# Optimization experiments

Measured on AMD Instinct MI355X. Metric: run time of the kernel, lower is better.

Reference implementation:

```python
import jax, jax.numpy as jnp
import numpy as np

B, N, H, DH, CZ = 1, 768, 16, 32, 128
D = H * DH  # 512
EPS = 1e-5


def layer_norm(x, w, b):
    mu = jnp.mean(x, axis=-1, keepdims=True)
    var = jnp.var(x, axis=-1, keepdims=True)
    return (x - mu) * jax.lax.rsqrt(var + EPS) * w + b


def setup_inputs() -> dict:
    key = jax.random.key(0)
    ks = jax.random.split(key, 10)
    sc = 0.02
    return {
        "s": jax.random.normal(ks[0], (B, N, D), jnp.float32),
        "z": jax.random.normal(ks[1], (B, N, N, CZ), jnp.float32),
        "norm_s_w": jnp.ones((D,), jnp.float32),
        "norm_s_b": jnp.zeros((D,), jnp.float32),
        "q_w": jax.random.normal(ks[2], (D, D), jnp.float32) * sc,
        "q_b": jax.random.normal(ks[3], (D,), jnp.float32) * sc,
        "k_w": jax.random.normal(ks[4], (D, D), jnp.float32) * sc,
        "v_w": jax.random.normal(ks[5], (D, D), jnp.float32) * sc,
        "g_w": jax.random.normal(ks[6], (D, D), jnp.float32) * sc,
        "zn_w": jnp.ones((CZ,), jnp.float32),
        "zn_b": jnp.zeros((CZ,), jnp.float32),
        "z_w": jax.random.normal(ks[7], (CZ, H), jnp.float32) * sc,
        "o_w": jax.random.normal(ks[8], (D, D), jnp.float32) * sc,
    }


def reference(s, z, norm_s_w, norm_s_b, q_w, q_b, k_w, v_w, g_w, zn_w, zn_b, z_w, o_w):
    # initial_norm on s
    s_n = layer_norm(s, norm_s_w, norm_s_b)
    # QKV projections (q has bias, k/v do not)
    q = (s_n @ q_w + q_b).reshape(B, N, H, DH)
    k = (s_n @ k_w).reshape(B, N, H, DH)
    v = (s_n @ v_w).reshape(B, N, H, DH)
    # attention scores [B, H, N, N]
    scores = jnp.einsum("bihd,bjhd->bhij", q, k) * (DH ** -0.5)
    # pair bias: layernorm(z) then linear c_z -> H, permute to [B, H, N, N]
    z_bias = layer_norm(z, zn_w, zn_b) @ z_w            # [B, N, N, H]
    z_bias = jnp.transpose(z_bias, (0, 3, 1, 2))         # [B, H, N, N]
    a = jax.nn.softmax(scores + z_bias, axis=-1)
    # attend
    o = jnp.einsum("bhij,bjhd->bihd", a, v).reshape(B, N, D)
    # sigmoid gate from normed s
    g = jax.nn.sigmoid(s_n @ g_w)
    # output projection
    return (o * g) @ o_w
```

## Files before the change

### kernel.cpp

```cpp
#include <hip/hip_runtime.h>
#include <hip/hip_bf16.h>

typedef float f32x4 __attribute__((ext_vector_type(4)));
typedef short bf16x8 __attribute__((ext_vector_type(8)));
typedef unsigned short u16;

#define NTOK 768
#define DMOD 512
#define NH   16
#define DH   32
#define CZd  128
#define NN   (768*768)

static __device__ __forceinline__ u16 f2bf(float f) {
  __hip_bfloat16 h = __float2bfloat16(f);
  return __builtin_bit_cast(u16, h);
}
static __device__ __forceinline__ float bf2f(u16 u) {
  unsigned int x = ((unsigned int)u) << 16;
  return __builtin_bit_cast(float, x);
}

__global__ __launch_bounds__(256) void prep_kernel(
    const float* __restrict__ s, const float* __restrict__ nsw, const float* __restrict__ nsb,
    const float* __restrict__ qw, const float* __restrict__ kw, const float* __restrict__ vw,
    const float* __restrict__ gw, const float* __restrict__ ow,
    const float* __restrict__ z, const float* __restrict__ znw, const float* __restrict__ znb,
    const float* __restrict__ zwp,
    u16* __restrict__ wbf, u16* __restrict__ snb, u16* __restrict__ biasb) {
  __shared__ char SM[17408];
  int bid = blockIdx.x;
  int t = threadIdx.x;

  if (bid >= 9216) {
    if (bid < 10496) {
      float (*tbuf)[33] = (float(*)[33])SM;
      int wb = bid - 9216;
      int seg = wb / 256;
      int tile = wb % 256;
      int k0 = (tile / 16) * 32;
      int n0 = (tile % 16) * 32;
      const float* src = seg==0?qw: seg==1?kw: seg==2?vw: seg==3?gw: ow;
      u16* out = wbf + (size_t)seg * (DMOD*DMOD);
      int tr  = t / 8;
      int tc4 = (t % 8) * 4;
      float4 v = *(const float4*)(src + (size_t)(k0+tr)*DMOD + n0 + tc4);
      tbuf[tr][tc4+0]=v.x; tbuf[tr][tc4+1]=v.y; tbuf[tr][tc4+2]=v.z; tbuf[tr][tc4+3]=v.w;
      __syncthreads();
      int nr  = t / 8;
      int kc4 = (t % 8) * 4;
      ushort4 o;
      o.x = f2bf(tbuf[kc4+0][nr]);
      o.y = f2bf(tbuf[kc4+1][nr]);
      o.z = f2bf(tbuf[kc4+2][nr]);
      o.w = f2bf(tbuf[kc4+3][nr]);
      *(ushort4*)(out + (size_t)(n0+nr)*DMOD + k0 + kc4) = o;
    } else {
      int i = (bid - 10496)*4 + (t >> 6);
      int lane = t & 63;
      const float* row = s + (size_t)i*DMOD + lane*8;
      float4 a0 = *(const float4*)(row);
      float4 a1 = *(const float4*)(row + 4);
      float sum = a0.x+a0.y+a0.z+a0.w + a1.x+a1.y+a1.z+a1.w;
      float sq  = a0.x*a0.x+a0.y*a0.y+a0.z*a0.z+a0.w*a0.w
                + a1.x*a1.x+a1.y*a1.y+a1.z*a1.z+a1.w*a1.w;
      #pragma unroll
      for (int mk=1; mk<64; mk<<=1) { sum += __shfl_xor(sum,mk); sq += __shfl_xor(sq,mk); }
      float mu  = sum * (1.f/512.f);
      float var = sq  * (1.f/512.f) - mu*mu;
      float rs  = rsqrtf(var + 1e-5f);
      float4 w0 = *(const float4*)(nsw + lane*8);
      float4 w1 = *(const float4*)(nsw + lane*8 + 4);
      float4 b0 = *(const float4*)(nsb + lane*8);
      float4 b1 = *(const float4*)(nsb + lane*8 + 4);
      bf16x8 o;
      o[0]=(short)f2bf((a0.x-mu)*rs*w0.x+b0.x);
      o[1]=(short)f2bf((a0.y-mu)*rs*w0.y+b0.y);
      o[2]=(short)f2bf((a0.z-mu)*rs*w0.z+b0.z);
      o[3]=(short)f2bf((a0.w-mu)*rs*w0.w+b0.w);
      o[4]=(short)f2bf((a1.x-mu)*rs*w1.x+b1.x);
      o[5]=(short)f2bf((a1.y-mu)*rs*w1.y+b1.y);
      o[6]=(short)f2bf((a1.z-mu)*rs*w1.z+b1.z);
      o[7]=(short)f2bf((a1.w-mu)*rs*w1.w+b1.w);
      *(bf16x8*)(snb + (size_t)i*DMOD + lane*8) = o;
    }
    return;
  }

  u16* zt = (u16*)SM;
  int i = bid / 12, j0 = (bid % 12) * 64;
  int lane = t & 63, wv = t >> 6;
  int c16 = lane & 15, c4 = lane >> 4;
  int rsub = t >> 5;
  int ch4  = (t & 31) * 4;
  const float* ztile = z + ((size_t)i*NTOK + j0)*CZd;
  float4 xv[8];
  #pragma unroll
  for (int it=0; it<8; it++)
    xv[it] = *(const float4*)(ztile + (size_t)(it*8 + rsub)*CZd + ch4);
  bf16x8 bfr[4];
  #pragma unroll
  for (int ks=0; ks<4; ks++) {
    #pragma unroll
    for (int jj=0; jj<8; jj++)
      bfr[ks][jj] = (short)f2bf(zwp[(ks*32 + c4*8 + jj)*16 + c16]);
  }
  float4 w4 = *(const float4*)(znw + ch4);
  float4 b4 = *(const float4*)(znb + ch4);
  float mu8[8], rs8[8];
  #pragma unroll
  for (int it=0; it<8; it++) {
    float4 v = xv[it];
    float sum = v.x+v.y+v.z+v.w;
    float sq  = v.x*v.x+v.y*v.y+v.z*v.z+v.w*v.w;
    #pragma unroll
    for (int mk=1; mk<32; mk<<=1) { sum += __shfl_xor(sum,mk); sq += __shfl_xor(sq,mk); }
    float mu = sum*(1.f/128.f);
    mu8[it] = mu;
    rs8[it] = rsqrtf(sq*(1.f/128.f) - mu*mu + 1e-5f);
  }
  #pragma unroll
  for (int it=0; it<8; it++) {
    float4 v = xv[it];
    float mu = mu8[it], rs = rs8[it];
    ushort4 o;
    o.x = f2bf((v.x-mu)*rs*w4.x + b4.x);
    o.y = f2bf((v.y-mu)*rs*w4.y + b4.y);
    o.z = f2bf((v.z-mu)*rs*w4.z + b4.z);
    o.w = f2bf((v.w-mu)*rs*w4.w + b4.w);
    *(ushort4*)(zt + (it*8 + rsub)*136 + ch4) = o;
  }
  __syncthreads();
  f32x4 acc = {0,0,0,0};
  #pragma unroll
  for (int ks=0; ks<4; ks++) {
    bf16x8 af = *(const bf16x8*)(zt + (wv*16 + c16)*136 + ks*32 + c4*8);
    acc = __builtin_amdgcn_mfma_f32_16x16x32_bf16(af, bfr[ks], acc, 0,0,0);
  }
  int jl = j0 + wv*16 + c4*4;
  u16* bp = biasb + ((size_t)i*NH + c16)*NTOK + jl;
  ushort4 st;
  st.x = f2bf(acc[0]); st.y = f2bf(acc[1]); st.z = f2bf(acc[2]); st.w = f2bf(acc[3]);
  *(ushort4*)bp = st;
}

__global__ __launch_bounds__(256) void qkvg_kernel(
    const u16* __restrict__ sn, const u16* __restrict__ wts, const float* __restrict__ qb,
    u16* __restrict__ qo, u16* __restrict__ ko, u16* __restrict__ vTo, float* __restrict__ go) {
  int bid = blockIdx.x;
  int mb = bid % 24, nb = bid / 24;
  int wsel = nb >> 3, n0 = (nb & 7) * 64, m0 = mb * 32;
  const u16* wt = wts + (size_t)wsel * (DMOD*DMOD);
  int t = threadIdx.x, lane = t & 63, wv = t >> 6;
  int wm = (wv >> 1) * 16, wn = (wv & 1) * 32;
  int c16 = lane & 15, c4 = lane >> 4;
  const u16* arow  = sn + (size_t)(m0 + wm + c16)*DMOD + c4*8;
  const u16* brow0 = wt + (size_t)(n0 + wn + c16)*DMOD + c4*8;
  const u16* brow1 = wt + (size_t)(n0 + wn + 16 + c16)*DMOD + c4*8;
  f32x4 acc0={0,0,0,0}, acc1={0,0,0,0};
  #pragma unroll 4
  for (int k0 = 0; k0 < DMOD; k0 += 32) {
    bf16x8 a  = *(const bf16x8*)(arow  + k0);
    bf16x8 b0 = *(const bf16x8*)(brow0 + k0);
    bf16x8 b1 = *(const bf16x8*)(brow1 + k0);
    acc0 = __builtin_amdgcn_mfma_f32_16x16x32_bf16(a,b0,acc0,0,0,0);
    acc1 = __builtin_amdgcn_mfma_f32_16x16x32_bf16(a,b1,acc1,0,0,0);
  }
  int r0 = c4*4;
  #pragma unroll
  for (int bn=0; bn<2; bn++) {
    f32x4 acc = bn==0?acc0:acc1;
    #pragma unroll
    for (int rr=0; rr<4; rr++) {
      int i = m0 + wm + r0 + rr;
      int n = n0 + wn + bn*16 + c16;
      float val = acc[rr];
      if (wsel == 0)      { val += qb[n]; qo[(size_t)i*DMOD + n] = f2bf(val); }
      else if (wsel == 1) { ko[(size_t)i*DMOD + n] = f2bf(val); }
      else if (wsel == 2) { vTo[(size_t)n*NTOK + i] = f2bf(val); }
      else                { go[(size_t)i*DMOD + n] = 1.f/(1.f + expf(-val)); }
    }
  }
}

__global__ __launch_bounds__(256) void attn_kernel(
    const u16* __restrict__ qm, const u16* __restrict__ km, const u16* __restrict__ vTm,
    const u16* __restrict__ bias, const float* __restrict__ gm, u16* __restrict__ og) {
  __shared__ u16 Pt[4][16*72];
  __shared__ float OS[4][16][33];
  __shared__ float LS[4][16];
  int h  = blockIdx.x & 15;
  int i0 = (blockIdx.x >> 4) * 16;
  int t = threadIdx.x, lane = t & 63, wv = t >> 6;
  int c16 = lane & 15, c4 = lane >> 4, r0 = c4 * 4;
  bf16x8 qf = *(const bf16x8*)(qm + (size_t)(i0 + c16)*DMOD + h*DH + c4*8);
  f32x4 o0 = {0,0,0,0}, o1 = {0,0,0,0};
  float ls[4] = {0.f,0.f,0.f,0.f};
  const float scale = 0.17677669529663687f;
  const u16* bbase = bias + ((size_t)i0*NH + h)*NTOK;
  u16* pt = &Pt[wv][0];
  for (int jj = 0; jj < 3; jj++) {
    int j0 = wv*192 + jj*64;
    bf16x8 kf0 = *(const bf16x8*)(km + (size_t)(j0 +  0 + c16)*DMOD + h*DH + c4*8);
    bf16x8 kf1 = *(const bf16x8*)(km + (size_t)(j0 + 16 + c16)*DMOD + h*DH + c4*8);
    bf16x8 kf2 = *(const bf16x8*)(km + (size_t)(j0 + 32 + c16)*DMOD + h*DH + c4*8);
    bf16x8 kf3 = *(const bf16x8*)(km + (size_t)(j0 + 48 + c16)*DMOD + h*DH + c4*8);
    f32x4 zz = {0,0,0,0};
    f32x4 s0 = __builtin_amdgcn_mfma_f32_16x16x32_bf16(qf,kf0,zz,0,0,0);
    f32x4 s1 = __builtin_amdgcn_mfma_f32_16x16x32_bf16(qf,kf1,zz,0,0,0);
    f32x4 s2 = __builtin_amdgcn_mfma_f32_16x16x32_bf16(qf,kf2,zz,0,0,0);
    f32x4 s3 = __builtin_amdgcn_mfma_f32_16x16x32_bf16(qf,kf3,zz,0,0,0);
    #pragma unroll
    for (int rr=0; rr<4; rr++) {
      const u16* bp = bbase + (size_t)(r0+rr)*(NH*NTOK) + j0 + c16;
      int row = (r0 + rr) * 72;
      float p0 = __expf(s0[rr]*scale + bf2f(bp[ 0]));
      float p1 = __expf(s1[rr]*scale + bf2f(bp[16]));
      float p2 = __expf(s2[rr]*scale + bf2f(bp[32]));
      float p3 = __expf(s3[rr]*scale + bf2f(bp[48]));
      ls[rr] += p0 + p1 + p2 + p3;
      pt[row + 0*16 + c16] = f2bf(p0);
      pt[row + 1*16 + c16] = f2bf(p1);
      pt[row + 2*16 + c16] = f2bf(p2);
      pt[row + 3*16 + c16] = f2bf(p3);
    }
    #pragma unroll
    for (int ks=0; ks<2; ks++) {
      bf16x8 pf = *(const bf16x8*)(pt + c16*72 + ks*32 + c4*8);
      bf16x8 v0 = *(const bf16x8*)(vTm + (size_t)(h*DH + c16)*NTOK      + j0 + ks*32 + c4*8);
      bf16x8 v1 = *(const bf16x8*)(vTm + (size_t)(h*DH + 16 + c16)*NTOK + j0 + ks*32 + c4*8);
      o0 = __builtin_amdgcn_mfma_f32_16x16x32_bf16(pf, v0, o0, 0,0,0);
      o1 = __builtin_amdgcn_mfma_f32_16x16x32_bf16(pf, v1, o1, 0,0,0);
    }
  }
  #pragma unroll
  for (int rr=0; rr<4; rr++) {
    float l = ls[rr];
    l += __shfl_xor(l,1); l += __shfl_xor(l,2); l += __shfl_xor(l,4); l += __shfl_xor(l,8);
    OS[wv][r0+rr][c16]      = o0[rr];
    OS[wv][r0+rr][16 + c16] = o1[rr];
    if (c16 == 0) LS[wv][r0+rr] = l;
  }
  __syncthreads();
  #pragma unroll
  for (int u=0; u<2; u++) {
    int idx = t + u*256;
    int row = idx >> 5, d = idx & 31;
    float osum = OS[0][row][d] + OS[1][row][d] + OS[2][row][d] + OS[3][row][d];
    float lsum = LS[0][row] + LS[1][row] + LS[2][row] + LS[3][row];
    int i = i0 + row;
    float g = gm[(size_t)i*DMOD + h*DH + d];
    og[(size_t)i*DMOD + h*DH + d] = f2bf(osum/lsum*g);
  }
}

__global__ __launch_bounds__(256) void out_kernel(
    const u16* __restrict__ og, const u16* __restrict__ owT, float* __restrict__ out) {
  int bid = blockIdx.x;
  int mb = bid % 24, nb = bid / 24;
  int m0 = mb*32, n0 = nb*64;
  int t = threadIdx.x, lane = t & 63, wv = t >> 6;
  int wm = (wv >> 1) * 16, wn = (wv & 1) * 32;
  int c16 = lane & 15, c4 = lane >> 4;
  const u16* arow  = og  + (size_t)(m0 + wm + c16)*DMOD + c4*8;
  const u16* brow0 = owT + (size_t)(n0 + wn + c16)*DMOD + c4*8;
  const u16* brow1 = owT + (size_t)(n0 + wn + 16 + c16)*DMOD + c4*8;
  f32x4 acc0={0,0,0,0}, acc1={0,0,0,0};
  #pragma unroll 4
  for (int k0 = 0; k0 < DMOD; k0 += 32) {
    bf16x8 a  = *(const bf16x8*)(arow  + k0);
    bf16x8 b0 = *(const bf16x8*)(brow0 + k0);
    bf16x8 b1 = *(const bf16x8*)(brow1 + k0);
    acc0 = __builtin_amdgcn_mfma_f32_16x16x32_bf16(a,b0,acc0,0,0,0);
    acc1 = __builtin_amdgcn_mfma_f32_16x16x32_bf16(a,b1,acc1,0,0,0);
  }
  int r0 = c4*4;
  #pragma unroll
  for (int bn=0; bn<2; bn++) {
    f32x4 acc = bn==0?acc0:acc1;
    #pragma unroll
    for (int rr=0; rr<4; rr++)
      out[(size_t)(m0 + wm + r0 + rr)*DMOD + n0 + wn + bn*16 + c16] = acc[rr];
  }
}

extern "C" void kernel_launch(void* const* d_in, const int* in_sizes, int n_in,
                              void* d_out, int out_size, void* d_ws, size_t ws_size,
                              hipStream_t stream) {
  const float* s   = (const float*)d_in[0];
  const float* z   = (const float*)d_in[1];
  const float* nsw = (const float*)d_in[2];
  const float* nsb = (const float*)d_in[3];
  const float* qw  = (const float*)d_in[4];
  const float* qb  = (const float*)d_in[5];
  const float* kw  = (const float*)d_in[6];
  const float* vw  = (const float*)d_in[7];
  const float* gw  = (const float*)d_in[8];
  const float* znw = (const float*)d_in[9];
  const float* znb = (const float*)d_in[10];
  const float* zw  = (const float*)d_in[11];
  const float* ow  = (const float*)d_in[12];
  float* out = (float*)d_out;

  char* p = (char*)d_ws;
  u16* w_bf    = (u16*)p;  p += (size_t)5*DMOD*DMOD*2;
  u16* sn_bf   = (u16*)p;  p += (size_t)NTOK*DMOD*2;
  u16* q_bf    = (u16*)p;  p += (size_t)NTOK*DMOD*2;
  u16* k_bf    = (u16*)p;  p += (size_t)NTOK*DMOD*2;
  u16* vT_bf   = (u16*)p;  p += (size_t)NTOK*DMOD*2;
  float* g_f   = (float*)p; p += (size_t)NTOK*DMOD*4;
  u16* og_bf   = (u16*)p;  p += (size_t)NTOK*DMOD*2;
  u16* bias_bf = (u16*)p;  p += (size_t)NH*NN*2;

  prep_kernel<<<dim3(10688), dim3(256), 0, stream>>>(
      s, nsw, nsb, qw, kw, vw, gw, ow, z, znw, znb, zw, w_bf, sn_bf, bias_bf);
  qkvg_kernel<<<dim3(768), dim3(256), 0, stream>>>(sn_bf, w_bf, qb, q_bf, k_bf, vT_bf, g_f);
  attn_kernel<<<dim3(768), dim3(256), 0, stream>>>(q_bf, k_bf, vT_bf, bias_bf, g_f, og_bf);
  out_kernel<<<dim3(192), dim3(256), 0, stream>>>(og_bf, w_bf + (size_t)4*DMOD*DMOD, out);
}
```

Baseline: 102.5 us.

## Process two z tiles per prep block and stage bias via LDS in attention

The pair-bias part of prep_kernel now handles two 64-column z tiles per block, issuing the loads for the second tile before the first tile's MFMA so they overlap. It reuses the converted z_w fragments across both tiles and halves the block count, at the cost of doubled LDS and more registers. In attn_kernel the bias loads become 16-byte vector loads into an LDS tile, replacing scattered 2-byte global loads, which adds LDS traffic and capacity pressure.

Result: no change. 102.4 us (-0.1%).

```diff
diff --git a/kernel.cpp b/kernel.cpp
--- a/kernel.cpp
+++ b/kernel.cpp
@@ -28,20 +28,20 @@
     const float* __restrict__ z, const float* __restrict__ znw, const float* __restrict__ znb,
     const float* __restrict__ zwp,
     u16* __restrict__ wbf, u16* __restrict__ snb, u16* __restrict__ biasb) {
-  __shared__ char SM[17408];
+  __shared__ __align__(16) char SM[34816];
   int bid = blockIdx.x;
   int t = threadIdx.x;
 
-  if (bid >= 9216) {
-    if (bid < 10496) {
+  if (bid >= 4608) {
+    if (bid < 5888) {
       float (*tbuf)[33] = (float(*)[33])SM;
-      int wb = bid - 9216;
+      int wb = bid - 4608;
       int seg = wb / 256;
       int tile = wb % 256;
       int k0 = (tile / 16) * 32;
       int n0 = (tile % 16) * 32;
       const float* src = seg==0?qw: seg==1?kw: seg==2?vw: seg==3?gw: ow;
-      u16* out = wbf + (size_t)seg * (DMOD*DMOD);
+      u16* outw = wbf + (size_t)seg * (DMOD*DMOD);
       int tr  = t / 8;
       int tc4 = (t % 8) * 4;
       float4 v = *(const float4*)(src + (size_t)(k0+tr)*DMOD + n0 + tc4);
@@ -54,9 +54,9 @@
       o.y = f2bf(tbuf[kc4+1][nr]);
       o.z = f2bf(tbuf[kc4+2][nr]);
       o.w = f2bf(tbuf[kc4+3][nr]);
-      *(ushort4*)(out + (size_t)(n0+nr)*DMOD + k0 + kc4) = o;
+      *(ushort4*)(outw + (size_t)(n0+nr)*DMOD + k0 + kc4) = o;
     } else {
-      int i = (bid - 10496)*4 + (t >> 6);
+      int i = (bid - 5888)*4 + (t >> 6);
       int lane = t & 63;
       const float* row = s + (size_t)i*DMOD + lane*8;
       float4 a0 = *(const float4*)(row);
@@ -87,17 +87,22 @@
     return;
   }
 
-  u16* zt = (u16*)SM;
-  int i = bid / 12, j0 = (bid % 12) * 64;
+  u16* zt0 = (u16*)SM;
+  u16* zt1 = (u16*)(SM + 17408);
+  int u0 = bid * 2;
+  int i  = u0 / 12;
+  int j0 = (u0 % 12) * 64;
   int lane = t & 63, wv = t >> 6;
   int c16 = lane & 15, c4 = lane >> 4;
   int rsub = t >> 5;
   int ch4  = (t & 31) * 4;
-  const float* ztile = z + ((size_t)i*NTOK + j0)*CZd;
+  const float* ztA = z + ((size_t)i*NTOK + j0)*CZd;
+  const float* ztB = ztA + (size_t)64*CZd;
+
   float4 xv[8];
   #pragma unroll
   for (int it=0; it<8; it++)
-    xv[it] = *(const float4*)(ztile + (size_t)(it*8 + rsub)*CZd + ch4);
+    xv[it] = *(const float4*)(ztA + (size_t)(it*8 + rsub)*CZd + ch4);
   bf16x8 bfr[4];
   #pragma unroll
   for (int ks=0; ks<4; ks++) {
@@ -107,41 +112,89 @@
   }
   float4 w4 = *(const float4*)(znw + ch4);
   float4 b4 = *(const float4*)(znb + ch4);
-  float mu8[8], rs8[8];
-  #pragma unroll
-  for (int it=0; it<8; it++) {
-    float4 v = xv[it];
-    float sum = v.x+v.y+v.z+v.w;
-    float sq  = v.x*v.x+v.y*v.y+v.z*v.z+v.w*v.w;
-    #pragma unroll
-    for (int mk=1; mk<32; mk<<=1) { sum += __shfl_xor(sum,mk); sq += __shfl_xor(sq,mk); }
-    float mu = sum*(1.f/128.f);
-    mu8[it] = mu;
-    rs8[it] = rsqrtf(sq*(1.f/128.f) - mu*mu + 1e-5f);
-  }
-  #pragma unroll
-  for (int it=0; it<8; it++) {
-    float4 v = xv[it];
-    float mu = mu8[it], rs = rs8[it];
-    ushort4 o;
-    o.x = f2bf((v.x-mu)*rs*w4.x + b4.x);
-    o.y = f2bf((v.y-mu)*rs*w4.y + b4.y);
-    o.z = f2bf((v.z-mu)*rs*w4.z + b4.z);
-    o.w = f2bf((v.w-mu)*rs*w4.w + b4.w);
-    *(ushort4*)(zt + (it*8 + rsub)*136 + ch4) = o;
-  }
+
+  {
+    float mu8[8], rs8[8];
+    #pragma unroll
+    for (int it=0; it<8; it++) {
+      float4 v = xv[it];
+      float sum = v.x+v.y+v.z+v.w;
+      float sq  = v.x*v.x+v.y*v.y+v.z*v.z+v.w*v.w;
+      #pragma unroll
+      for (int mk=1; mk<32; mk<<=1) { sum += __shfl_xor(sum,mk); sq += __shfl_xor(sq,mk); }
+      float mu = sum*(1.f/128.f);
+      mu8[it] = mu;
+      rs8[it] = rsqrtf(sq*(1.f/128.f) - mu*mu + 1e-5f);
+    }
+    #pragma unroll
+    for (int it=0; it<8; it++) {
+      float4 v = xv[it];
+      float mu = mu8[it], rs = rs8[it];
+      ushort4 o;
+      o.x = f2bf((v.x-mu)*rs*w4.x + b4.x);
+      o.y = f2bf((v.y-mu)*rs*w4.y + b4.y);
+      o.z = f2bf((v.z-mu)*rs*w4.z + b4.z);
+      o.w = f2bf((v.w-mu)*rs*w4.w + b4.w);
+      *(ushort4*)(zt0 + (it*8 + rsub)*136 + ch4) = o;
+    }
+  }
+  float4 yv[8];
+  #pragma unroll
+  for (int it=0; it<8; it++)
+    yv[it] = *(const float4*)(ztB + (size_t)(it*8 + rsub)*CZd + ch4);
   __syncthreads();
-  f32x4 acc = {0,0,0,0};
-  #pragma unroll
-  for (int ks=0; ks<4; ks++) {
-    bf16x8 af = *(const bf16x8*)(zt + (wv*16 + c16)*136 + ks*32 + c4*8);
-    acc = __builtin_amdgcn_mfma_f32_16x16x32_bf16(af, bfr[ks], acc, 0,0,0);
-  }
-  int jl = j0 + wv*16 + c4*4;
-  u16* bp = biasb + ((size_t)i*NH + c16)*NTOK + jl;
-  ushort4 st;
-  st.x = f2bf(acc[0]); st.y = f2bf(acc[1]); st.z = f2bf(acc[2]); st.w = f2bf(acc[3]);
-  *(ushort4*)bp = st;
+  {
+    f32x4 acc = {0,0,0,0};
+    #pragma unroll
+    for (int ks=0; ks<4; ks++) {
+      bf16x8 af = *(const bf16x8*)(zt0 + (wv*16 + c16)*136 + ks*32 + c4*8);
+      acc = __builtin_amdgcn_mfma_f32_16x16x32_bf16(af, bfr[ks], acc, 0,0,0);
+    }
+    int jl = j0 + wv*16 + c4*4;
+    u16* bp = biasb + ((size_t)i*NH + c16)*NTOK + jl;
+    ushort4 st;
+    st.x = f2bf(acc[0]); st.y = f2bf(acc[1]); st.z = f2bf(acc[2]); st.w = f2bf(acc[3]);
+    *(ushort4*)bp = st;
+  }
+  {
+    float mu8[8], rs8[8];
+    #pragma unroll
+    for (int it=0; it<8; it++) {
+      float4 v = yv[it];
+      float sum = v.x+v.y+v.z+v.w;
+      float sq  = v.x*v.x+v.y*v.y+v.z*v.z+v.w*v.w;
+      #pragma unroll
+      for (int mk=1; mk<32; mk<<=1) { sum += __shfl_xor(sum,mk); sq += __shfl_xor(sq,mk); }
+      float mu = sum*(1.f/128.f);
+      mu8[it] = mu;
+      rs8[it] = rsqrtf(sq*(1.f/128.f) - mu*mu + 1e-5f);
+    }
+    #pragma unroll
+    for (int it=0; it<8; it++) {
+      float4 v = yv[it];
+      float mu = mu8[it], rs = rs8[it];
+      ushort4 o;
+      o.x = f2bf((v.x-mu)*rs*w4.x + b4.x);
+      o.y = f2bf((v.y-mu)*rs*w4.y + b4.y);
+      o.z = f2bf((v.z-mu)*rs*w4.z + b4.z);
+      o.w = f2bf((v.w-mu)*rs*w4.w + b4.w);
+      *(ushort4*)(zt1 + (it*8 + rsub)*136 + ch4) = o;
+    }
+  }
+  __syncthreads();
+  {
+    f32x4 acc = {0,0,0,0};
+    #pragma unroll
+    for (int ks=0; ks<4; ks++) {
+      bf16x8 af = *(const bf16x8*)(zt1 + (wv*16 + c16)*136 + ks*32 + c4*8);
+      acc = __builtin_amdgcn_mfma_f32_16x16x32_bf16(af, bfr[ks], acc, 0,0,0);
+    }
+    int jl = j0 + 64 + wv*16 + c4*4;
+    u16* bp = biasb + ((size_t)i*NH + c16)*NTOK + jl;
+    ushort4 st;
+    st.x = f2bf(acc[0]); st.y = f2bf(acc[1]); st.z = f2bf(acc[2]); st.w = f2bf(acc[3]);
+    *(ushort4*)bp = st;
+  }
 }
 
 __global__ __launch_bounds__(256) void qkvg_kernel(
@@ -186,6 +239,7 @@
 __global__ __launch_bounds__(256) void attn_kernel(
     const u16* __restrict__ qm, const u16* __restrict__ km, const u16* __restrict__ vTm,
     const u16* __restrict__ bias, const float* __restrict__ gm, u16* __restrict__ og) {
+  __shared__ u16 Bt[4][16*72];
   __shared__ u16 Pt[4][16*72];
   __shared__ float OS[4][16][33];
   __shared__ float LS[4][16];
@@ -198,13 +252,20 @@
   float ls[4] = {0.f,0.f,0.f,0.f};
   const float scale = 0.17677669529663687f;
   const u16* bbase = bias + ((size_t)i0*NH + h)*NTOK;
+  int br = lane >> 3;
+  int bc = (lane & 7) * 8;
+  u16* bt = &Bt[wv][0];
   u16* pt = &Pt[wv][0];
   for (int jj = 0; jj < 3; jj++) {
     int j0 = wv*192 + jj*64;
+    bf16x8 bv0 = *(const bf16x8*)(bbase + (size_t)br*(NH*NTOK)     + j0 + bc);
+    bf16x8 bv1 = *(const bf16x8*)(bbase + (size_t)(br+8)*(NH*NTOK) + j0 + bc);
     bf16x8 kf0 = *(const bf16x8*)(km + (size_t)(j0 +  0 + c16)*DMOD + h*DH + c4*8);
     bf16x8 kf1 = *(const bf16x8*)(km + (size_t)(j0 + 16 + c16)*DMOD + h*DH + c4*8);
     bf16x8 kf2 = *(const bf16x8*)(km + (size_t)(j0 + 32 + c16)*DMOD + h*DH + c4*8);
     bf16x8 kf3 = *(const bf16x8*)(km + (size_t)(j0 + 48 + c16)*DMOD + h*DH + c4*8);
+    *(bf16x8*)(bt + br*72 + bc)     = bv0;
+    *(bf16x8*)(bt + (br+8)*72 + bc) = bv1;
     f32x4 zz = {0,0,0,0};
     f32x4 s0 = __builtin_amdgcn_mfma_f32_16x16x32_bf16(qf,kf0,zz,0,0,0);
     f32x4 s1 = __builtin_amdgcn_mfma_f32_16x16x32_bf16(qf,kf1,zz,0,0,0);
@@ -212,12 +273,11 @@
     f32x4 s3 = __builtin_amdgcn_mfma_f32_16x16x32_bf16(qf,kf3,zz,0,0,0);
     #pragma unroll
     for (int rr=0; rr<4; rr++) {
-      const u16* bp = bbase + (size_t)(r0+rr)*(NH*NTOK) + j0 + c16;
       int row = (r0 + rr) * 72;
-      float p0 = __expf(s0[rr]*scale + bf2f(bp[ 0]));
-      float p1 = __expf(s1[rr]*scale + bf2f(bp[16]));
-      float p2 = __expf(s2[rr]*scale + bf2f(bp[32]));
-      float p3 = __expf(s3[rr]*scale + bf2f(bp[48]));
+      float p0 = __expf(s0[rr]*scale + bf2f(bt[row + 0*16 + c16]));
+      float p1 = __expf(s1[rr]*scale + bf2f(bt[row + 1*16 + c16]));
+      float p2 = __expf(s2[rr]*scale + bf2f(bt[row + 2*16 + c16]));
+      float p3 = __expf(s3[rr]*scale + bf2f(bt[row + 3*16 + c16]));
       ls[rr] += p0 + p1 + p2 + p3;
       pt[row + 0*16 + c16] = f2bf(p0);
       pt[row + 1*16 + c16] = f2bf(p1);
@@ -312,7 +372,7 @@
   u16* og_bf   = (u16*)p;  p += (size_t)NTOK*DMOD*2;
   u16* bias_bf = (u16*)p;  p += (size_t)NH*NN*2;
 
-  prep_kernel<<<dim3(10688), dim3(256), 0, stream>>>(
+  prep_kernel<<<dim3(6080), dim3(256), 0, stream>>>(
       s, nsw, nsb, qw, kw, vw, gw, ow, z, znw, znb, zw, w_bf, sn_bf, bias_bf);
   qkvg_kernel<<<dim3(768), dim3(256), 0, stream>>>(sn_bf, w_bf, qb, q_bf, k_bf, vT_bf, g_f);
   attn_kernel<<<dim3(768), dim3(256), 0, stream>>>(q_bf, k_bf, vT_bf, bias_bf, g_f, og_bf);
```
